# Optimization experiments

Hardware: AMD Instinct MI355X
Metric: run time of the kernel (lower is better)

## Reference

```python
import jax, jax.numpy as jnp
import numpy as np

N, E, M = 8192, 32768, 2048
D, H1, C = 768, 8, 768
NEG_SLOPE = 0.2


def gat_conv(x, src, dst, W, att_src, att_dst, bias, heads, out_ch):
    # PyG GATConv (eval mode, concat=True, add_self_loops already applied to src/dst)
    n = x.shape[0]
    h = (x @ W).reshape(n, heads, out_ch)                      # [N,H,C]
    a_src = jnp.einsum('nhc,hc->nh', h, att_src)               # [N,H]
    a_dst = jnp.einsum('nhc,hc->nh', h, att_dst)
    e = jax.nn.leaky_relu(a_src[src] + a_dst[dst], NEG_SLOPE)  # [E',H]
    # softmax over incoming edges of each dst node
    m = jax.ops.segment_max(e, dst, num_segments=n)
    e = jnp.exp(e - m[dst])
    denom = jax.ops.segment_sum(e, dst, num_segments=n)
    alpha = e / (denom[dst] + 1e-16)                           # [E',H]
    msg = h[src] * alpha[:, :, None]                           # [E',H,C]
    out = jax.ops.segment_sum(msg, dst, num_segments=n)        # [N,H,C]
    return out.reshape(n, heads * out_ch) + bias


def setup_inputs() -> dict:
    key = jax.random.key(0)
    ks = jax.random.split(key, 16)
    s = 0.02
    inp = {
        'x': jax.random.normal(ks[0], (N, D), jnp.float32),
        'edge_index': jax.random.randint(ks[1], (2, E), 0, N, jnp.int64),
        'mask_idx': jax.random.randint(ks[2], (M,), 0, N, jnp.int64),
        'W1': jax.random.normal(ks[3], (D, H1 * C), jnp.float32) * s,
        'att_src1': jax.random.normal(ks[4], (H1, C), jnp.float32) * s,
        'att_dst1': jax.random.normal(ks[5], (H1, C), jnp.float32) * s,
        'b1': jnp.zeros((H1 * C,), jnp.float32),
        'W2': jax.random.normal(ks[6], (H1 * C, C), jnp.float32) * s,
        'att_src2': jax.random.normal(ks[7], (1, C), jnp.float32) * s,
        'att_dst2': jax.random.normal(ks[8], (1, C), jnp.float32) * s,
        'b2': jnp.zeros((C,), jnp.float32),
        # fc: 1536 -> 768, classifier: 768 -> 2
        'fc_w': jax.random.normal(ks[9], (2 * C, C), jnp.float32) * s,
        'fc_b': jnp.zeros((C,), jnp.float32),
        'cls_w': jax.random.normal(ks[10], (C, 2), jnp.float32) * s,
        'cls_b': jnp.zeros((2,), jnp.float32),
    }
    return inp


def reference(x, edge_index, mask_idx, W1, att_src1, att_dst1, b1,
              W2, att_src2, att_dst2, b2, fc_w, fc_b, cls_w, cls_b):
    n = x.shape[0]
    loops = jnp.arange(n, dtype=edge_index.dtype)
    src = jnp.concatenate([edge_index[0], loops])   # PyG default add_self_loops
    dst = jnp.concatenate([edge_index[1], loops])
    h = gat_conv(x, src, dst, W1, att_src1, att_dst1, b1, H1, C)   # [N, 6144]
    h = jax.nn.elu(h)
    h = gat_conv(h, src, dst, W2, att_src2, att_dst2, b2, 1, C)    # [N, 768]
    x_gemb = h[mask_idx]                                           # [M, 768]
    x_emb = x[mask_idx]                                            # [M, 768]
    out = jnp.concatenate([x_gemb, x_emb], axis=1) @ fc_w + fc_b   # [M, 768]
    out = out @ cls_w + cls_b                                      # [M, 2]
    return out
```

## Files before the change

### kernel.cpp

```cpp
#include <hip/hip_runtime.h>

typedef unsigned short ushort_t;
typedef __attribute__((ext_vector_type(8))) __bf16 bf16x8;
typedef __attribute__((ext_vector_type(8))) unsigned short ushort8;
typedef __attribute__((ext_vector_type(4))) unsigned short ushort4v;
typedef __attribute__((ext_vector_type(4))) float f32x4;

#define N_NODES 8192
#define NODE_MASK 8191
#define E_EDGES 32768
#define E_TOT   40960
#define M_MASK  2048
#define D_IN    768
#define C_CH    768
#define F1      6144

typedef __attribute__((address_space(1))) const void* gas_ptr;
typedef __attribute__((address_space(3))) void* las_ptr;

__device__ __forceinline__ float bf2f(ushort_t u) {
    union { unsigned int i; float f; } v; v.i = ((unsigned int)u) << 16; return v.f;
}
__device__ __forceinline__ ushort_t f2bf(float f) {
    union { float f; unsigned int i; } v; v.f = f;
    unsigned int r = v.i + 0x7fffu + ((v.i >> 16) & 1u);
    return (ushort_t)(r >> 16);
}

__global__ void init_kernel(int* deg, int* fill, int* flags) {
    int i = blockIdx.x * 256 + threadIdx.x;
    if (i < N_NODES) { deg[i] = 0; fill[i] = 0; }
    if (i < 2) flags[i] = 0;
}
__global__ void detect_kernel(const int* __restrict__ raw, int nhalf, int* __restrict__ flag) {
    int i = blockIdx.x * 256 + threadIdx.x;
    if (i < nhalf && raw[2 * i + 1] != 0) atomicOr(flag, 1);
}
__global__ void convert_idx_kernel(const void* __restrict__ raw, int n,
                                   const int* __restrict__ flag, int* __restrict__ out) {
    int i = blockIdx.x * 256 + threadIdx.x;
    if (i >= n) return;
    int v = (*flag) ? ((const int*)raw)[i] : (int)((const long long*)raw)[i];
    out[i] = v & NODE_MASK;
}

__global__ void cvt_bf16_kernel(const float* __restrict__ in, ushort_t* __restrict__ out, int n4) {
    int i = blockIdx.x * 256 + threadIdx.x;
    if (i >= n4) return;
    f32x4 v = *(const f32x4*)(in + i * 4);
    ushort_t o0 = f2bf(v[0]), o1 = f2bf(v[1]), o2 = f2bf(v[2]), o3 = f2bf(v[3]);
    unsigned long long pk = (unsigned long long)o0 | ((unsigned long long)o1 << 16)
                          | ((unsigned long long)o2 << 32) | ((unsigned long long)o3 << 48);
    *(unsigned long long*)(out + i * 4) = pk;
}

__global__ __launch_bounds__(256) void transpose_cvt_kernel(
    const float* __restrict__ in, ushort_t* __restrict__ out, int R, int Ccols)
{
    __shared__ ushort_t tile[32][33];
    int tx = threadIdx.x & 31, ty = threadIdx.x >> 5;
    int x  = blockIdx.x * 32 + tx;
    int y0 = blockIdx.y * 32;
#pragma unroll
    for (int i = 0; i < 4; ++i)
        tile[ty + i * 8][tx] = f2bf(in[(size_t)(y0 + ty + i * 8) * Ccols + x]);
    __syncthreads();
#pragma unroll
    for (int i = 0; i < 4; ++i)
        out[(size_t)(blockIdx.x * 32 + ty + i * 8) * R + y0 + tx] = tile[tx][ty + i * 8];
}

__global__ __launch_bounds__(256) void gemm_bt_kernel(
    const ushort_t* __restrict__ A, const ushort_t* __restrict__ Bt,
    ushort_t* __restrict__ C, const float* __restrict__ bias,
    int M, int N, int K)
{
    __shared__ ushort_t lsA[128 * 64];
    __shared__ ushort_t lsB[128 * 64];

    const int tid  = threadIdx.x;
    const int lane = tid & 63;
    const int wave = tid >> 6;
    const int wm = wave >> 1, wn = wave & 1;

    const int GX = gridDim.x, GY = gridDim.y;
    const int lin = blockIdx.y * GX + blockIdx.x;
    const int byg = (GY >= 8) ? (GY >> 3) : 1;
    const int xcd = lin & 7;
    const int jj  = lin >> 3;
    const int bx  = jj / byg;
    const int by  = (GY >= 8) ? (xcd * byg + (jj % byg)) : blockIdx.y;

    const f32x4 zero = {0.f, 0.f, 0.f, 0.f};
    f32x4 acc[4][4];
#pragma unroll
    for (int i = 0; i < 4; ++i)
#pragma unroll
        for (int j = 0; j < 4; ++j) acc[i][j] = zero;

    const int l8 = lane >> 3;
    const int c8 = lane & 7;
    const int q  = lane >> 4;
    const int rl = lane & 15;

    for (int kt = 0; kt < K; kt += 64) {
        __syncthreads();
#pragma unroll
        for (int i = 0; i < 4; ++i) {
            int rbase = wave * 32 + i * 8;
            int row   = rbase + l8;
            int gch   = c8 ^ (row & 7);
            const ushort_t* gA = A  + (size_t)(by * 128 + row) * K + kt + gch * 8;
            const ushort_t* gB = Bt + (size_t)(bx * 128 + row) * K + kt + gch * 8;
            __builtin_amdgcn_global_load_lds((gas_ptr)gA, (las_ptr)(lsA + rbase * 64), 16, 0, 0);
            __builtin_amdgcn_global_load_lds((gas_ptr)gB, (las_ptr)(lsB + rbase * 64), 16, 0, 0);
        }
        __syncthreads();
#pragma unroll
        for (int s = 0; s < 2; ++s) {
            bf16x8 af[4], bfv[4];
#pragma unroll
            for (int i = 0; i < 4; ++i) {
                int Ra = wm * 64 + i * 16 + rl;
                af[i]  = *(const bf16x8*)(lsA + Ra * 64 + (((s * 4 + q) ^ (Ra & 7)) * 8));
                int Rb = wn * 64 + i * 16 + rl;
                bfv[i] = *(const bf16x8*)(lsB + Rb * 64 + (((s * 4 + q) ^ (Rb & 7)) * 8));
            }
#pragma unroll
            for (int i = 0; i < 4; ++i)
#pragma unroll
                for (int j = 0; j < 4; ++j)
                    acc[i][j] = __builtin_amdgcn_mfma_f32_16x16x32_bf16(af[i], bfv[j], acc[i][j], 0, 0, 0);
        }
    }
#pragma unroll
    for (int j = 0; j < 4; ++j) {
        int col = bx * 128 + wn * 64 + j * 16 + rl;
        float bv = bias ? bias[col] : 0.0f;
#pragma unroll
        for (int i = 0; i < 4; ++i) {
#pragma unroll
            for (int t = 0; t < 4; ++t) {
                int row = by * 128 + wm * 64 + i * 16 + q * 4 + t;
                C[(size_t)row * N + col] = f2bf(acc[i][j][t] + bv);
            }
        }
    }
}

__global__ void indeg_kernel(const int* __restrict__ eic, int* __restrict__ deg) {
    int e = blockIdx.x * 256 + threadIdx.x;
    if (e >= E_TOT) return;
    int dst = (e < E_EDGES) ? eic[E_EDGES + e] : (e - E_EDGES);
    atomicAdd(&deg[dst], 1);
}
__global__ __launch_bounds__(256) void scan_kernel(const int* __restrict__ deg, int* __restrict__ rowptr) {
    __shared__ int part[256];
    int t = threadIdx.x;
    int local[32];
    int s = 0;
#pragma unroll
    for (int i = 0; i < 32; ++i) { local[i] = deg[t * 32 + i]; s += local[i]; }
    part[t] = s;
    __syncthreads();
    for (int off = 1; off < 256; off <<= 1) {
        int v = (t >= off) ? part[t - off] : 0;
        __syncthreads();
        part[t] += v;
        __syncthreads();
    }
    int run = (t == 0) ? 0 : part[t - 1];
#pragma unroll
    for (int i = 0; i < 32; ++i) { rowptr[t * 32 + i] = run; run += local[i]; }
    if (t == 255) rowptr[N_NODES] = run;
}
__global__ void scatter_kernel(const int* __restrict__ eic, const int* __restrict__ rowptr,
                               int* __restrict__ fill, int* __restrict__ csr_src) {
    int e = blockIdx.x * 256 + threadIdx.x;
    if (e >= E_TOT) return;
    int src, dst;
    if (e < E_EDGES) { src = eic[e]; dst = eic[E_EDGES + e]; }
    else             { src = e - E_EDGES; dst = src; }
    int pos = rowptr[dst] + atomicAdd(&fill[dst], 1);
    csr_src[pos] = src;
}

__global__ __launch_bounds__(256) void att_kernel(
    const ushort_t* __restrict__ h, const float* __restrict__ att_s,
    const float* __restrict__ att_d, float* __restrict__ a_s, float* __restrict__ a_d,
    int heads, int stride)
{
    int gid  = blockIdx.x * 4 + (threadIdx.x >> 6);
    int lane = threadIdx.x & 63;
    int n = gid / heads, hd = gid % heads;
    const ushort_t* hp = h + (size_t)n * stride + hd * C_CH;
    const float* sp = att_s + hd * C_CH;
    const float* dp = att_d + hd * C_CH;
    float s1 = 0.f, s2 = 0.f;
#pragma unroll
    for (int j = 0; j < 3; ++j) {
        int o = j * 256 + lane * 4;
        ushort4v hv = *(const ushort4v*)(hp + o);
        f32x4 sv = *(const f32x4*)(sp + o);
        f32x4 dv = *(const f32x4*)(dp + o);
#pragma unroll
        for (int k = 0; k < 4; ++k) {
            float f = bf2f(hv[k]);
            s1 += f * sv[k];
            s2 += f * dv[k];
        }
    }
#pragma unroll
    for (int off = 32; off > 0; off >>= 1) {
        s1 += __shfl_down(s1, off);
        s2 += __shfl_down(s2, off);
    }
    if (lane == 0) { a_s[gid] = s1; a_d[gid] = s2; }
}

__global__ __launch_bounds__(192) void agg8_kernel(
    const ushort_t* __restrict__ h, const float* __restrict__ a_s, const float* __restrict__ a_d,
    const int* __restrict__ rowptr, const int* __restrict__ csr_src,
    const float* __restrict__ bias, ushort_t* __restrict__ out)
{
    const int n = blockIdx.x;
    const int half = blockIdx.y;
    const int tid = threadIdx.x;
    const int base = rowptr[n];
    const int deg  = rowptr[n + 1] - base;

    __shared__ float s_m[8], s_rd[8], s_adst[8];
    __shared__ int   s_src[64];
    __shared__ float s_w[64][8];

    if (tid < 8) {
        float adst = a_d[n * 8 + tid];
        float m = -1e30f;
        for (int e = 0; e < deg; ++e) {
            float scv = a_s[csr_src[base + e] * 8 + tid] + adst;
            scv = scv > 0.f ? scv : 0.2f * scv;
            m = fmaxf(m, scv);
        }
        float den = 0.f;
        for (int e = 0; e < deg; ++e) {
            float scv = a_s[csr_src[base + e] * 8 + tid] + adst;
            scv = scv > 0.f ? scv : 0.2f * scv;
            den += __expf(scv - m);
        }
        s_m[tid] = m; s_rd[tid] = 1.0f / (den + 1e-16f); s_adst[tid] = adst;
    }
    __syncthreads();

    float acc[16];
#pragma unroll
    for (int i = 0; i < 16; ++i) acc[i] = 0.f;
    const int c0   = half * 3072 + tid * 16;
    const int myhd = (half << 2) + tid / 48;

    for (int cs = 0; cs < deg; cs += 64) {
        int cnt = min(64, deg - cs);
        __syncthreads();
        for (int idx = tid; idx < cnt; idx += 192) s_src[idx] = csr_src[base + cs + idx];
        __syncthreads();
        for (int idx = tid; idx < cnt * 8; idx += 192) {
            int e = idx >> 3, hd = idx & 7;
            float scv = a_s[s_src[e] * 8 + hd] + s_adst[hd];
            scv = scv > 0.f ? scv : 0.2f * scv;
            s_w[e][hd] = __expf(scv - s_m[hd]) * s_rd[hd];
        }
        __syncthreads();
        int e = 0;
        for (; e + 3 < cnt; e += 4) {
            const ushort_t* p0 = h + (size_t)s_src[e]     * F1 + c0;
            const ushort_t* p1 = h + (size_t)s_src[e + 1] * F1 + c0;
            const ushort_t* p2 = h + (size_t)s_src[e + 2] * F1 + c0;
            const ushort_t* p3 = h + (size_t)s_src[e + 3] * F1 + c0;
            ushort8 a0 = *(const ushort8*)(p0), a1 = *(const ushort8*)(p0 + 8);
            ushort8 b0 = *(const ushort8*)(p1), b1 = *(const ushort8*)(p1 + 8);
            ushort8 c0v = *(const ushort8*)(p2), c1v = *(const ushort8*)(p2 + 8);
            ushort8 d0 = *(const ushort8*)(p3), d1 = *(const ushort8*)(p3 + 8);
            float w0 = s_w[e][myhd], w1 = s_w[e + 1][myhd];
            float w2 = s_w[e + 2][myhd], w3 = s_w[e + 3][myhd];
#pragma unroll
            for (int i = 0; i < 8; ++i) {
                acc[i]     += w0 * bf2f(a0[i]) + w1 * bf2f(b0[i]) + w2 * bf2f(c0v[i]) + w3 * bf2f(d0[i]);
                acc[8 + i] += w0 * bf2f(a1[i]) + w1 * bf2f(b1[i]) + w2 * bf2f(c1v[i]) + w3 * bf2f(d1[i]);
            }
        }
        for (; e < cnt; ++e) {
            const ushort_t* p0 = h + (size_t)s_src[e] * F1 + c0;
            ushort8 a0 = *(const ushort8*)(p0), a1 = *(const ushort8*)(p0 + 8);
            float w0 = s_w[e][myhd];
#pragma unroll
            for (int i = 0; i < 8; ++i) {
                acc[i]     += w0 * bf2f(a0[i]);
                acc[8 + i] += w0 * bf2f(a1[i]);
            }
        }
    }
#pragma unroll
    for (int i = 0; i < 16; ++i) {
        float v = acc[i] + bias[c0 + i];
        v = v > 0.f ? v : (__expf(v) - 1.0f);
        out[(size_t)n * F1 + c0 + i] = f2bf(v);
    }
}

__global__ __launch_bounds__(256) void agg1_kernel(
    const ushort_t* __restrict__ h, const float* __restrict__ a_s, const float* __restrict__ a_d,
    const int* __restrict__ rowptr, const int* __restrict__ csr_src,
    const float* __restrict__ bias, ushort_t* __restrict__ out)
{
    const int n = blockIdx.x;
    const int tid = threadIdx.x;
    const int base = rowptr[n];
    const int deg  = rowptr[n + 1] - base;
    __shared__ float s_m, s_rd, s_adst;
    __shared__ int   s_src[64];
    __shared__ float s_w[64];
    if (tid == 0) {
        float adst = a_d[n];
        float m = -1e30f;
        for (int e = 0; e < deg; ++e) {
            float scv = a_s[csr_src[base + e]] + adst;
            scv = scv > 0.f ? scv : 0.2f * scv;
            m = fmaxf(m, scv);
        }
        float den = 0.f;
        for (int e = 0; e < deg; ++e) {
            float scv = a_s[csr_src[base + e]] + adst;
            scv = scv > 0.f ? scv : 0.2f * scv;
            den += __expf(scv - m);
        }
        s_m = m; s_rd = 1.0f / (den + 1e-16f); s_adst = adst;
    }
    __syncthreads();
    float acc0 = 0.f, acc1 = 0.f, acc2 = 0.f;
    const int c0 = tid * 3;
    for (int cs = 0; cs < deg; cs += 64) {
        int cnt = min(64, deg - cs);
        __syncthreads();
        for (int idx = tid; idx < cnt; idx += 256) s_src[idx] = csr_src[base + cs + idx];
        __syncthreads();
        for (int idx = tid; idx < cnt; idx += 256) {
            float scv = a_s[s_src[idx]] + s_adst;
            scv = scv > 0.f ? scv : 0.2f * scv;
            s_w[idx] = __expf(scv - s_m) * s_rd;
        }
        __syncthreads();
        for (int e = 0; e < cnt; ++e) {
            const ushort_t* hp = h + (size_t)s_src[e] * C_CH + c0;
            float w = s_w[e];
            acc0 += w * bf2f(hp[0]);
            acc1 += w * bf2f(hp[1]);
            acc2 += w * bf2f(hp[2]);
        }
    }
    out[(size_t)n * C_CH + c0 + 0] = f2bf(acc0 + bias[c0 + 0]);
    out[(size_t)n * C_CH + c0 + 1] = f2bf(acc1 + bias[c0 + 1]);
    out[(size_t)n * C_CH + c0 + 2] = f2bf(acc2 + bias[c0 + 2]);
}

__global__ void gatherfc_kernel(const ushort_t* __restrict__ out2, const ushort_t* __restrict__ xb,
                                const int* __restrict__ maskc, ushort_t* __restrict__ Afc)
{
    int m = blockIdx.x, t = threadIdx.x;
    int mi = maskc[m];
    const ushort4v* p1 = (const ushort4v*)(out2 + (size_t)mi * 768);
    const ushort4v* p2 = (const ushort4v*)(xb   + (size_t)mi * 768);
    ushort4v* q1 = (ushort4v*)(Afc + (size_t)m * 1536);
    ushort4v* q2 = (ushort4v*)(Afc + (size_t)m * 1536 + 768);
    if (t < 192) { q1[t] = p1[t]; q2[t] = p2[t]; }
}

__global__ __launch_bounds__(256) void cls_kernel(
    const ushort_t* __restrict__ fc_out, const float* __restrict__ cls_w,
    const float* __restrict__ cls_b, float* __restrict__ out)
{
    int m = blockIdx.x * 4 + (threadIdx.x >> 6);
    int lane = threadIdx.x & 63;
    float a0 = 0.f, a1 = 0.f;
    const ushort_t* row = fc_out + (size_t)m * 768;
    for (int i = lane; i < 768; i += 64) {
        float v = bf2f(row[i]);
        a0 += v * cls_w[i * 2 + 0];
        a1 += v * cls_w[i * 2 + 1];
    }
#pragma unroll
    for (int off = 32; off > 0; off >>= 1) {
        a0 += __shfl_down(a0, off);
        a1 += __shfl_down(a1, off);
    }
    if (lane == 0) {
        out[m * 2 + 0] = a0 + cls_b[0];
        out[m * 2 + 1] = a1 + cls_b[1];
    }
}

extern "C" void kernel_launch(void* const* d_in, const int* in_sizes, int n_in,
                              void* d_out, int out_size, void* d_ws, size_t ws_size,
                              hipStream_t stream)
{
    const float* x        = (const float*)d_in[0];
    const void*  ei_raw   = d_in[1];
    const void*  mask_raw = d_in[2];
    const float* W1       = (const float*)d_in[3];
    const float* att_src1 = (const float*)d_in[4];
    const float* att_dst1 = (const float*)d_in[5];
    const float* b1       = (const float*)d_in[6];
    const float* W2       = (const float*)d_in[7];
    const float* att_src2 = (const float*)d_in[8];
    const float* att_dst2 = (const float*)d_in[9];
    const float* b2       = (const float*)d_in[10];
    const float* fc_w     = (const float*)d_in[11];
    const float* fc_b     = (const float*)d_in[12];
    const float* cls_w    = (const float*)d_in[13];
    const float* cls_b    = (const float*)d_in[14];
    float* out = (float*)d_out;

    char* ws = (char*)d_ws;
    size_t off = 0;
    auto alloc = [&](size_t bytes) { char* p = ws + off; off = (off + bytes + 255) & ~(size_t)255; return p; };
    int*   flags  = (int*)alloc(2 * 4);
    int*   eic    = (int*)alloc((size_t)2 * E_EDGES * 4);
    int*   maskc  = (int*)alloc((size_t)M_MASK * 4);
    int*   deg    = (int*)alloc(N_NODES * 4);
    int*   fill   = (int*)alloc(N_NODES * 4);
    int*   rowptr = (int*)alloc((N_NODES + 1) * 4);
    int*   csr    = (int*)alloc(E_TOT * 4);
    float* a_s1   = (float*)alloc((size_t)N_NODES * 8 * 4);
    float* a_d1   = (float*)alloc((size_t)N_NODES * 8 * 4);
    float* a_s2   = (float*)alloc((size_t)N_NODES * 4);
    float* a_d2   = (float*)alloc((size_t)N_NODES * 4);
    ushort_t* W1t  = (ushort_t*)alloc((size_t)D_IN * F1 * 2);
    ushort_t* W2t  = (ushort_t*)alloc((size_t)F1 * C_CH * 2);
    ushort_t* fcwt = (ushort_t*)alloc((size_t)1536 * 768 * 2);
    ushort_t* xb   = (ushort_t*)alloc((size_t)N_NODES * D_IN * 2);
    char* region1 = alloc((size_t)N_NODES * F1 * 2);
    char* region2 = alloc((size_t)N_NODES * F1 * 2);
    ushort_t* h1    = (ushort_t*)region1;
    ushort_t* h2    = (ushort_t*)region1;
    ushort_t* Afc   = (ushort_t*)(region1 + (16u << 20));
    ushort_t* fcout = (ushort_t*)(region1 + (32u << 20));
    ushort_t* out1  = (ushort_t*)region2;
    ushort_t* out2  = (ushort_t*)region2;

    init_kernel<<<N_NODES / 256, 256, 0, stream>>>(deg, fill, flags);
    detect_kernel<<<(E_EDGES + 255) / 256, 256, 0, stream>>>((const int*)ei_raw, E_EDGES, &flags[0]);
    detect_kernel<<<(M_MASK / 2 + 255) / 256, 256, 0, stream>>>((const int*)mask_raw, M_MASK / 2, &flags[1]);
    convert_idx_kernel<<<(2 * E_EDGES + 255) / 256, 256, 0, stream>>>(ei_raw, 2 * E_EDGES, &flags[0], eic);
    convert_idx_kernel<<<(M_MASK + 255) / 256, 256, 0, stream>>>(mask_raw, M_MASK, &flags[1], maskc);
    indeg_kernel<<<E_TOT / 256, 256, 0, stream>>>(eic, deg);
    scan_kernel<<<1, 256, 0, stream>>>(deg, rowptr);
    scatter_kernel<<<E_TOT / 256, 256, 0, stream>>>(eic, rowptr, fill, csr);

    cvt_bf16_kernel<<<(N_NODES * D_IN / 4 + 255) / 256, 256, 0, stream>>>(x, xb, N_NODES * D_IN / 4);
    transpose_cvt_kernel<<<dim3(F1 / 32, D_IN / 32), 256, 0, stream>>>(W1, W1t, D_IN, F1);
    transpose_cvt_kernel<<<dim3(C_CH / 32, F1 / 32), 256, 0, stream>>>(W2, W2t, F1, C_CH);
    transpose_cvt_kernel<<<dim3(768 / 32, 1536 / 32), 256, 0, stream>>>(fc_w, fcwt, 1536, 768);

    gemm_bt_kernel<<<dim3(F1 / 128, N_NODES / 128), 256, 0, stream>>>(xb, W1t, h1, nullptr, N_NODES, F1, D_IN);
    att_kernel<<<(N_NODES * 8) / 4, 256, 0, stream>>>(h1, att_src1, att_dst1, a_s1, a_d1, 8, F1);
    agg8_kernel<<<dim3(N_NODES, 2), 192, 0, stream>>>(h1, a_s1, a_d1, rowptr, csr, b1, out1);

    gemm_bt_kernel<<<dim3(C_CH / 128, N_NODES / 128), 256, 0, stream>>>(out1, W2t, h2, nullptr, N_NODES, C_CH, F1);
    att_kernel<<<N_NODES / 4, 256, 0, stream>>>(h2, att_src2, att_dst2, a_s2, a_d2, 1, C_CH);
    agg1_kernel<<<N_NODES, 256, 0, stream>>>(h2, a_s2, a_d2, rowptr, csr, b2, out2);

    gatherfc_kernel<<<M_MASK, 256, 0, stream>>>(out2, xb, maskc, Afc);
    gemm_bt_kernel<<<dim3(768 / 128, M_MASK / 128), 256, 0, stream>>>(Afc, fcwt, fcout, fc_b, M_MASK, 768, 1536);
    cls_kernel<<<M_MASK / 4, 256, 0, stream>>>(fcout, cls_w, cls_b, out);
}
```

Measured before the change: 562.2 us.

## Split-K the second GAT and fc GEMMs with fused reduction epilogues

The second-layer GEMM and the fc GEMM are launched with a 4-way K split, each slice writing fp32 partials. A new kernel sums the layer-2 partials, converts them to bf16 and computes the attention logits in one pass, replacing the separate att kernel. The classifier kernel now reduces the fc partials and adds the bias itself. This raises block count to fill the GPU better, at the cost of extra fp32 partial traffic through memory.

New measurement: 553.3 us. About the same (-1.6%).

```diff
diff --git a/kernel.cpp b/kernel.cpp
--- a/kernel.cpp
+++ b/kernel.cpp
@@ -73,7 +73,8 @@
 __global__ __launch_bounds__(256) void gemm_bt_kernel(
     const ushort_t* __restrict__ A, const ushort_t* __restrict__ Bt,
     ushort_t* __restrict__ C, const float* __restrict__ bias,
-    int M, int N, int K)
+    float* __restrict__ Cp,
+    int M, int N, int K, int k0, int ksz)
 {
     __shared__ ushort_t lsA[128 * 64];
     __shared__ ushort_t lsB[128 * 64];
@@ -88,7 +89,7 @@
     const int byg = (GY >= 8) ? (GY >> 3) : 1;
     const int xcd = lin & 7;
     const int jj  = lin >> 3;
-    const int bx  = jj / byg;
+    const int bx  = (GY >= 8) ? (jj / byg) : blockIdx.x;
     const int by  = (GY >= 8) ? (xcd * byg + (jj % byg)) : blockIdx.y;
 
     const f32x4 zero = {0.f, 0.f, 0.f, 0.f};
@@ -103,7 +104,8 @@
     const int q  = lane >> 4;
     const int rl = lane & 15;
 
-    for (int kt = 0; kt < K; kt += 64) {
+    const int kbeg = k0 + blockIdx.z * ksz;
+    for (int kt = kbeg; kt < kbeg + ksz; kt += 64) {
         __syncthreads();
 #pragma unroll
         for (int i = 0; i < 4; ++i) {
@@ -133,17 +135,31 @@
                     acc[i][j] = __builtin_amdgcn_mfma_f32_16x16x32_bf16(af[i], bfv[j], acc[i][j], 0, 0, 0);
         }
     }
-#pragma unroll
-    for (int j = 0; j < 4; ++j) {
-        int col = bx * 128 + wn * 64 + j * 16 + rl;
-        float bv = bias ? bias[col] : 0.0f;
-#pragma unroll
-        for (int i = 0; i < 4; ++i) {
-#pragma unroll
-            for (int t = 0; t < 4; ++t) {
-                int row = by * 128 + wm * 64 + i * 16 + q * 4 + t;
-                C[(size_t)row * N + col] = f2bf(acc[i][j][t] + bv);
-            }
+    if (Cp) {
+        float* Cpz = Cp + (size_t)blockIdx.z * M * N;
+#pragma unroll
+        for (int j = 0; j < 4; ++j) {
+            int col = bx * 128 + wn * 64 + j * 16 + rl;
+#pragma unroll
+            for (int i = 0; i < 4; ++i)
+#pragma unroll
+                for (int t = 0; t < 4; ++t) {
+                    int row = by * 128 + wm * 64 + i * 16 + q * 4 + t;
+                    Cpz[(size_t)row * N + col] = acc[i][j][t];
+                }
+        }
+    } else {
+#pragma unroll
+        for (int j = 0; j < 4; ++j) {
+            int col = bx * 128 + wn * 64 + j * 16 + rl;
+            float bv = bias ? bias[col] : 0.0f;
+#pragma unroll
+            for (int i = 0; i < 4; ++i)
+#pragma unroll
+                for (int t = 0; t < 4; ++t) {
+                    int row = by * 128 + wm * 64 + i * 16 + q * 4 + t;
+                    C[(size_t)row * N + col] = f2bf(acc[i][j][t] + bv);
+                }
         }
     }
 }
@@ -216,6 +232,36 @@
         s2 += __shfl_down(s2, off);
     }
     if (lane == 0) { a_s[gid] = s1; a_d[gid] = s2; }
+}
+
+__global__ __launch_bounds__(256) void cvtatt_kernel(
+    const float* __restrict__ Cp, ushort_t* __restrict__ h2,
+    const float* __restrict__ att_s, const float* __restrict__ att_d,
+    float* __restrict__ a_s, float* __restrict__ a_d)
+{
+    __shared__ float ps[4], pd[4];
+    const int n = blockIdx.x, t = threadIdx.x;
+    const size_t SL = (size_t)N_NODES * 768;
+    const float* row = Cp + (size_t)n * 768;
+    float v0 = row[t]       + row[SL + t]       + row[2 * SL + t]       + row[3 * SL + t];
+    float v1 = row[t + 256] + row[SL + t + 256] + row[2 * SL + t + 256] + row[3 * SL + t + 256];
+    float v2 = row[t + 512] + row[SL + t + 512] + row[2 * SL + t + 512] + row[3 * SL + t + 512];
+    h2[(size_t)n * 768 + t]       = f2bf(v0);
+    h2[(size_t)n * 768 + t + 256] = f2bf(v1);
+    h2[(size_t)n * 768 + t + 512] = f2bf(v2);
+    float s1 = v0 * att_s[t] + v1 * att_s[t + 256] + v2 * att_s[t + 512];
+    float s2 = v0 * att_d[t] + v1 * att_d[t + 256] + v2 * att_d[t + 512];
+#pragma unroll
+    for (int o = 32; o > 0; o >>= 1) {
+        s1 += __shfl_down(s1, o);
+        s2 += __shfl_down(s2, o);
+    }
+    if ((t & 63) == 0) { ps[t >> 6] = s1; pd[t >> 6] = s2; }
+    __syncthreads();
+    if (t == 0) {
+        a_s[n] = ps[0] + ps[1] + ps[2] + ps[3];
+        a_d[n] = pd[0] + pd[1] + pd[2] + pd[3];
+    }
 }
 
 __global__ __launch_bounds__(192) void agg8_kernel(
@@ -374,15 +420,17 @@
 }
 
 __global__ __launch_bounds__(256) void cls_kernel(
-    const ushort_t* __restrict__ fc_out, const float* __restrict__ cls_w,
-    const float* __restrict__ cls_b, float* __restrict__ out)
+    const float* __restrict__ fcp, const float* __restrict__ fc_b,
+    const float* __restrict__ cls_w, const float* __restrict__ cls_b,
+    float* __restrict__ out)
 {
     int m = blockIdx.x * 4 + (threadIdx.x >> 6);
     int lane = threadIdx.x & 63;
+    const size_t SL = (size_t)M_MASK * 768;
     float a0 = 0.f, a1 = 0.f;
-    const ushort_t* row = fc_out + (size_t)m * 768;
+    const float* row = fcp + (size_t)m * 768;
     for (int i = lane; i < 768; i += 64) {
-        float v = bf2f(row[i]);
+        float v = row[i] + row[SL + i] + row[2 * SL + i] + row[3 * SL + i] + fc_b[i];
         a0 += v * cls_w[i * 2 + 0];
         a1 += v * cls_w[i * 2 + 1];
     }
@@ -438,12 +486,13 @@
     ushort_t* xb   = (ushort_t*)alloc((size_t)N_NODES * D_IN * 2);
     char* region1 = alloc((size_t)N_NODES * F1 * 2);
     char* region2 = alloc((size_t)N_NODES * F1 * 2);
-    ushort_t* h1    = (ushort_t*)region1;
-    ushort_t* h2    = (ushort_t*)region1;
-    ushort_t* Afc   = (ushort_t*)(region1 + (16u << 20));
-    ushort_t* fcout = (ushort_t*)(region1 + (32u << 20));
-    ushort_t* out1  = (ushort_t*)region2;
-    ushort_t* out2  = (ushort_t*)region2;
+    ushort_t* h1  = (ushort_t*)region1;
+    float*    Cp  = (float*)region1;
+    float*    fcp = (float*)region1;
+    ushort_t* out1 = (ushort_t*)region2;
+    ushort_t* out2 = (ushort_t*)region2;
+    ushort_t* h2   = (ushort_t*)(region2 + (16u << 20));
+    ushort_t* Afc  = (ushort_t*)(region2 + (32u << 20));
 
     init_kernel<<<N_NODES / 256, 256, 0, stream>>>(deg, fill, flags);
     detect_kernel<<<(E_EDGES + 255) / 256, 256, 0, stream>>>((const int*)ei_raw, E_EDGES, &flags[0]);
@@ -459,15 +508,18 @@
     transpose_cvt_kernel<<<dim3(C_CH / 32, F1 / 32), 256, 0, stream>>>(W2, W2t, F1, C_CH);
     transpose_cvt_kernel<<<dim3(768 / 32, 1536 / 32), 256, 0, stream>>>(fc_w, fcwt, 1536, 768);
 
-    gemm_bt_kernel<<<dim3(F1 / 128, N_NODES / 128), 256, 0, stream>>>(xb, W1t, h1, nullptr, N_NODES, F1, D_IN);
+    gemm_bt_kernel<<<dim3(F1 / 128, N_NODES / 128), 256, 0, stream>>>(
+        xb, W1t, h1, nullptr, nullptr, N_NODES, F1, D_IN, 0, D_IN);
     att_kernel<<<(N_NODES * 8) / 4, 256, 0, stream>>>(h1, att_src1, att_dst1, a_s1, a_d1, 8, F1);
     agg8_kernel<<<dim3(N_NODES, 2), 192, 0, stream>>>(h1, a_s1, a_d1, rowptr, csr, b1, out1);
 
-    gemm_bt_kernel<<<dim3(C_CH / 128, N_NODES / 128), 256, 0, stream>>>(out1, W2t, h2, nullptr, N_NODES, C_CH, F1);
-    att_kernel<<<N_NODES / 4, 256, 0, stream>>>(h2, att_src2, att_dst2, a_s2, a_d2, 1, C_CH);
+    gemm_bt_kernel<<<dim3(C_CH / 128, N_NODES / 128, 4), 256, 0, stream>>>(
+        out1, W2t, nullptr, nullptr, Cp, N_NODES, C_CH, F1, 0, F1 / 4);
+    cvtatt_kernel<<<N_NODES, 256, 0, stream>>>(Cp, h2, att_src2, att_dst2, a_s2, a_d2);
     agg1_kernel<<<N_NODES, 256, 0, stream>>>(h2, a_s2, a_d2, rowptr, csr, b2, out2);
 
     gatherfc_kernel<<<M_MASK, 256, 0, stream>>>(out2, xb, maskc, Afc);
-    gemm_bt_kernel<<<dim3(768 / 128, M_MASK / 128), 256, 0, stream>>>(Afc, fcwt, fcout, fc_b, M_MASK, 768, 1536);
-    cls_kernel<<<M_MASK / 4, 256, 0, stream>>>(fcout, cls_w, cls_b, out);
-}
+    gemm_bt_kernel<<<dim3(768 / 128, M_MASK / 128, 4), 256, 0, stream>>>(
+        Afc, fcwt, nullptr, nullptr, fcp, M_MASK, 768, 1536, 0, 1536 / 4);
+    cls_kernel<<<M_MASK / 4, 256, 0, stream>>>(fcp, fc_b, cls_w, cls_b, out);
+}
```
